# Kernel tuning notes

Measured on AMD Instinct MI355X. Metric: run time of the kernel, lower is better.

## Reference

```python
import jax, jax.numpy as jnp
import numpy as np

DIM, K, H, D, G = 1024, 4, 8, 128, 4

def rotate_half(x):
    x1, x2 = jnp.split(x, 2, axis=-1)
    return jnp.concatenate([-x2, x1], axis=-1)

def setup_inputs() -> dict:
    key = jax.random.key(0)
    ks = jax.random.split(key, 14)
    s = 0.02
    return {
        "x":  jax.random.normal(ks[0], (1, 2048, DIM), jnp.float32),
        "Wq": jax.random.normal(ks[1], (H * D, DIM), jnp.float32) * s,
        "bq": jnp.zeros((H * D,), jnp.float32),
        "Wk": jax.random.normal(ks[2], (G * D, DIM), jnp.float32) * s,
        "bk": jnp.zeros((G * D,), jnp.float32),
        "Wv": jax.random.normal(ks[3], (G * D, DIM), jnp.float32) * s,
        "bv": jnp.zeros((G * D,), jnp.float32),
        "Wo": jax.random.normal(ks[4], (DIM, H * D), jnp.float32) * s,
        "bo": jnp.zeros((DIM,), jnp.float32),
        "W1": jax.random.normal(ks[5], (DIM * 4, DIM), jnp.float32) * s,
        "b1": jnp.zeros((DIM * 4,), jnp.float32),
        "W2": jax.random.normal(ks[6], (K * DIM, DIM * 4), jnp.float32) * s,
        "b2": jnp.zeros((K * DIM,), jnp.float32),
    }

def reference(x, Wq, bq, Wk, bk, Wv, bv, Wo, bo, W1, b1, W2, b2):
    B, S, _ = x.shape
    q = (x @ Wq.T + bq).reshape(B, S, H, D).transpose(0, 2, 1, 3)  # (B,H,S,D)
    k = (x @ Wk.T + bk).reshape(B, S, G, D).transpose(0, 2, 1, 3)  # (B,G,S,D)
    v = (x @ Wv.T + bv).reshape(B, S, G, D).transpose(0, 2, 1, 3)
    # rotary embedding (same as RotaryEmbedding module)
    inv_freq = 1.0 / (10000.0 ** (jnp.arange(0, D, 2, dtype=jnp.float32) / D))
    t = jnp.arange(S, dtype=jnp.float32)
    freqs = t[:, None] * inv_freq[None, :]
    emb = jnp.concatenate([freqs, freqs], axis=-1)            # (S, D)
    cos = jnp.cos(emb)[None, None, :, :]
    sin = jnp.sin(emb)[None, None, :, :]
    q = q * cos + rotate_half(q) * sin
    k = k * cos + rotate_half(k) * sin
    # every q head attends to every kv group; softmax over j, then sum over g and j
    scores = jnp.einsum('bhid,bgjd->bhgij', q, k) / jnp.sqrt(jnp.float32(D))
    mask = jnp.triu(jnp.ones((S, S), dtype=bool), 1)
    scores = jnp.where(mask[None, None, None, :, :], -jnp.inf, scores)
    w = jax.nn.softmax(scores, axis=-1)
    attn = jnp.einsum('bhgij,bgjd->bhid', w, v)               # (B,H,S,D)
    attn = attn.transpose(0, 2, 1, 3).reshape(B, S, H * D)
    o = attn @ Wo.T + bo
    h1 = jax.nn.silu(o @ W1.T + b1)
    out = (h1 @ W2.T + b2).reshape(B, S, K, DIM)
    return out
```

## Files before the change

### kernel.cpp

```cpp
#include <hip/hip_runtime.h>
#include <hip/hip_bf16.h>

#define SEQ 2048

typedef unsigned short ushort_t;
typedef __attribute__((ext_vector_type(8))) short short8;
typedef __attribute__((ext_vector_type(4))) float f32x4;

__device__ __forceinline__ ushort_t f2bf(float f) {
    __hip_bfloat16 h = __float2bfloat16(f);
    return *reinterpret_cast<ushort_t*>(&h);
}

__device__ __forceinline__ void st(float* p, float v) { *p = v; }
__device__ __forceinline__ void st(ushort_t* p, float v) { *p = f2bf(v); }

__device__ __forceinline__ void gload16(const ushort_t* g, ushort_t* l) {
    __builtin_amdgcn_global_load_lds(
        (const __attribute__((address_space(1))) unsigned int*)g,
        (__attribute__((address_space(3))) unsigned int*)l, 16, 0, 0);
}

__global__ void cvt_bf_kernel(const float* __restrict__ s0, ushort_t* __restrict__ d0, int n0,
                              const float* __restrict__ s1, ushort_t* __restrict__ d1, int n1,
                              const float* __restrict__ s2, ushort_t* __restrict__ d2, int n2,
                              const float* __restrict__ s3, ushort_t* __restrict__ d3, int n3,
                              const float* __restrict__ s4, ushort_t* __restrict__ d4) {
    int u = blockIdx.x * 256 + threadIdx.x;
    const float* s; ushort_t* d;
    if (u < n0) { s = s0; d = d0; }
    else if ((u -= n0) < n1) { s = s1; d = d1; }
    else if ((u -= n1) < n2) { s = s2; d = d2; }
    else if ((u -= n2) < n3) { s = s3; d = d3; }
    else { u -= n3; s = s4; d = d4; }
    float4 a = ((const float4*)s)[u];
    union { ushort_t us[4]; unsigned long long ll; } pk;
    pk.us[0] = f2bf(a.x); pk.us[1] = f2bf(a.y);
    pk.us[2] = f2bf(a.z); pk.us[3] = f2bf(a.w);
    ((unsigned long long*)d)[u] = pk.ll;
}

template <bool SILU, typename TC>
__global__ __launch_bounds__(256) void mfma_gemm_kernel(
    const ushort_t* __restrict__ A, const ushort_t* __restrict__ W,
    const float* __restrict__ bias0, const float* __restrict__ bias1,
    const float* __restrict__ bias2, int sp1, int sp2,
    TC* __restrict__ C, int M, int N, int Kd, int NBX) {
    __shared__ __align__(16) ushort_t As[128 * 64];
    __shared__ __align__(16) ushort_t Bs[128 * 64];
    const int tid = threadIdx.x;
    const int w = tid >> 6, lane = tid & 63, l15 = lane & 15, quad = lane >> 4;
    const int nwg = gridDim.x;
    const int qq = nwg >> 3;
    const int bid = blockIdx.x;
    const int sw = (bid & 7) * qq + (bid >> 3);
    const int m0 = (sw / NBX) * 128, n0 = (sw % NBX) * 128;
    const int rw = (w >> 1) * 64, cw = (w & 1) * 64;
    const int rA = w * 32 + (lane >> 3);
    const int cch = ((lane & 7) ^ (lane >> 3)) * 8;

    f32x4 acc[4][4];
#pragma unroll
    for (int mt = 0; mt < 4; ++mt)
#pragma unroll
        for (int nt = 0; nt < 4; ++nt) acc[mt][nt] = (f32x4){0.f, 0.f, 0.f, 0.f};

    for (int k0 = 0; k0 < Kd; k0 += 64) {
#pragma unroll
        for (int c = 0; c < 4; ++c) {
            gload16(&A[(size_t)(m0 + rA + c * 8) * Kd + k0 + cch],
                    &As[(w * 4 + c) * 512]);
            gload16(&W[(size_t)(n0 + rA + c * 8) * Kd + k0 + cch],
                    &Bs[(w * 4 + c) * 512]);
        }
        __syncthreads();
#pragma unroll
        for (int kc = 0; kc < 2; ++kc) {
            short8 af[4], bfr[4];
#pragma unroll
            for (int mt = 0; mt < 4; ++mt) {
                int row = rw + mt * 16 + l15;
                int slot = (kc * 4 + quad) ^ (row & 7);
                af[mt] = *(const short8*)&As[row * 64 + slot * 8];
            }
#pragma unroll
            for (int nt = 0; nt < 4; ++nt) {
                int row = cw + nt * 16 + l15;
                int slot = (kc * 4 + quad) ^ (row & 7);
                bfr[nt] = *(const short8*)&Bs[row * 64 + slot * 8];
            }
#pragma unroll
            for (int mt = 0; mt < 4; ++mt)
#pragma unroll
                for (int nt = 0; nt < 4; ++nt)
                    acc[mt][nt] = __builtin_amdgcn_mfma_f32_16x16x32_bf16(
                        af[mt], bfr[nt], acc[mt][nt], 0, 0, 0);
        }
        __syncthreads();
    }
#pragma unroll
    for (int nt = 0; nt < 4; ++nt) {
        int col = n0 + cw + nt * 16 + l15;
        float bb = col < sp1 ? bias0[col]
                 : (col < sp2 ? bias1[col - sp1] : bias2[col - sp2]);
#pragma unroll
        for (int mt = 0; mt < 4; ++mt)
#pragma unroll
            for (int r = 0; r < 4; ++r) {
                int row = m0 + rw + mt * 16 + quad * 4 + r;
                float v = acc[mt][nt][r] + bb;
                if (SILU) v = v / (1.f + __expf(-v));
                st(&C[(size_t)row * N + col], v);
            }
    }
}

__global__ void rope_bf_kernel(const float* __restrict__ qkv,
                               ushort_t* __restrict__ qb, ushort_t* __restrict__ kb) {
    const int s = blockIdx.x;
    const float t = (float)s;
    const float qs = 0.08838834764831845f;
    for (int p = threadIdx.x; p < 768; p += 256) {
        int idx = p & 63;
        float invf = exp2f(-(float)idx * 0.20762050593f);
        float ang = t * invf;
        float c = cosf(ang), sn = sinf(ang);
        if (p < 512) {
            int h = p >> 6;
            const float* src = qkv + (size_t)s * 2048 + h * 128 + idx;
            ushort_t* dst = qb + (size_t)s * 1024 + h * 128 + idx;
            float x1 = src[0], x2 = src[64];
            dst[0] = f2bf((x1 * c - x2 * sn) * qs);
            dst[64] = f2bf((x2 * c + x1 * sn) * qs);
        } else {
            int h = (p - 512) >> 6;
            const float* src = qkv + (size_t)s * 2048 + 1024 + h * 128 + idx;
            ushort_t* dst = kb + (size_t)s * 512 + h * 128 + idx;
            float x1 = src[0], x2 = src[64];
            dst[0] = f2bf(x1 * c - x2 * sn);
            dst[64] = f2bf(x2 * c + x1 * sn);
        }
    }
}

__global__ void transpose_v_kernel(const float* __restrict__ qkv, ushort_t* __restrict__ vT) {
    __shared__ __align__(16) ushort_t t[64][72];
    const int s0 = blockIdx.x * 64, d0 = blockIdx.y * 64;
    const int tid = threadIdx.x;
#pragma unroll
    for (int it = 0; it < 4; ++it) {
        int u = tid + it * 256;
        int r = u >> 4, c4 = u & 15;
        float4 a = *(const float4*)&qkv[(size_t)(s0 + r) * 2048 + 1536 + d0 + c4 * 4];
        union { ushort_t us[4]; unsigned long long ll; } pk;
        pk.us[0] = f2bf(a.x); pk.us[1] = f2bf(a.y);
        pk.us[2] = f2bf(a.z); pk.us[3] = f2bf(a.w);
        *(unsigned long long*)&t[r][c4 * 4] = pk.ll;
    }
    __syncthreads();
#pragma unroll
    for (int it = 0; it < 2; ++it) {
        int u = tid + it * 256;
        int r = u >> 3, c8 = u & 7;
        short8 o;
        ushort_t* op = (ushort_t*)&o;
#pragma unroll
        for (int i = 0; i < 8; ++i) op[i] = t[c8 * 8 + i][r];
        *(short8*)&vT[(size_t)(d0 + r) * 2048 + s0 + c8 * 8] = o;
    }
}

__global__ __launch_bounds__(256, 2) void mfma_attn_kernel(
    const ushort_t* __restrict__ qb, const ushort_t* __restrict__ kb,
    const ushort_t* __restrict__ vT, float* __restrict__ part) {
    const int tid = threadIdx.x;
    const int w = tid >> 6;
    const int lane = tid & 63;
    const int l15 = lane & 15;
    const int quad = lane >> 4;
    const int bx = blockIdx.x;
    const int pr = bx >> 3;
    const int g = (bx >> 1) & 3;
    const int h = (bx & 1) * 4 + w;

    const ushort_t* vtg = vT + (size_t)g * 128 * 2048;

    __shared__ __align__(16) ushort_t Ks[64 * 128];
    __shared__ __align__(16) ushort_t Vs[128 * 64];
    __shared__ __align__(16) ushort_t P_lds[4][16][72];

#pragma unroll 1
    for (int half = 0; half < 2; ++half) {
        const int p = half ? (127 - pr) : pr;
        const int i0 = p << 4;
        const int jmax = p >> 2;
        const int rbase = (p & 3) << 4;

        short8 aq[4];
        {
            const ushort_t* qrow = qb + (size_t)(i0 + l15) * 1024 + h * 128 + quad * 8;
#pragma unroll
            for (int kc = 0; kc < 4; ++kc) aq[kc] = *(const short8*)(qrow + kc * 32);
        }
        f32x4 oacc[8];
#pragma unroll
        for (int nt = 0; nt < 8; ++nt) oacc[nt] = (f32x4){0.f, 0.f, 0.f, 0.f};
        float l_part[4] = {0.f, 0.f, 0.f, 0.f};

        short8 kreg[4], vreg[4];
#pragma unroll
        for (int it = 0; it < 4; ++it) {
            int fl = it * 256 + tid;
            int r = fl >> 4, c8 = fl & 15;
            kreg[it] = *(const short8*)&kb[(size_t)r * 512 + g * 128 + c8 * 8];
        }
#pragma unroll
        for (int it = 0; it < 4; ++it) {
            int fl = it * 256 + tid;
            int r = fl >> 3, c8 = fl & 7;
            vreg[it] = *(const short8*)&vtg[(size_t)r * 2048 + c8 * 8];
        }

        for (int jt = 0; jt <= jmax; ++jt) {
            __syncthreads();
#pragma unroll
            for (int it = 0; it < 4; ++it) {
                int fl = it * 256 + tid;
                int r = fl >> 4, c8 = fl & 15;
                *(short8*)&Ks[r * 128 + ((c8 ^ (r & 7)) * 8)] = kreg[it];
            }
#pragma unroll
            for (int it = 0; it < 4; ++it) {
                int fl = it * 256 + tid;
                int r = fl >> 3, c8 = fl & 7;
                *(short8*)&Vs[r * 64 + ((c8 ^ (r & 7)) * 8)] = vreg[it];
            }
            __syncthreads();
            if (jt < jmax) {
                const int j1 = (jt + 1) << 6;
#pragma unroll
                for (int it = 0; it < 4; ++it) {
                    int fl = it * 256 + tid;
                    int r = fl >> 4, c8 = fl & 15;
                    kreg[it] = *(const short8*)&kb[(size_t)(j1 + r) * 512 + g * 128 + c8 * 8];
                }
#pragma unroll
                for (int it = 0; it < 4; ++it) {
                    int fl = it * 256 + tid;
                    int r = fl >> 3, c8 = fl & 7;
                    vreg[it] = *(const short8*)&vtg[(size_t)r * 2048 + j1 + c8 * 8];
                }
            }
            f32x4 sacc[4];
#pragma unroll
            for (int nt = 0; nt < 4; ++nt) sacc[nt] = (f32x4){0.f, 0.f, 0.f, 0.f};
#pragma unroll
            for (int nt = 0; nt < 4; ++nt) {
                const ushort_t* krow = &Ks[(nt * 16 + l15) * 128];
                const int sw = l15 & 7;
#pragma unroll
                for (int kc = 0; kc < 4; ++kc) {
                    short8 bk = *(const short8*)(krow + (((kc * 4 + quad) ^ sw) * 8));
                    sacc[nt] = __builtin_amdgcn_mfma_f32_16x16x32_bf16(
                        aq[kc], bk, sacc[nt], 0, 0, 0);
                }
            }
            if (jt == jmax) {
#pragma unroll
                for (int nt = 0; nt < 4; ++nt) {
                    int colg = nt * 16 + l15;
#pragma unroll
                    for (int r = 0; r < 4; ++r) {
                        int rowg = rbase + quad * 4 + r;
                        if (colg > rowg) sacc[nt][r] = -1e30f;
                    }
                }
            }
#pragma unroll
            for (int nt = 0; nt < 4; ++nt)
#pragma unroll
                for (int r = 0; r < 4; ++r) {
                    float e = __expf(sacc[nt][r] - 14.f);
                    sacc[nt][r] = e;
                    l_part[r] += e;
                }
#pragma unroll
            for (int nt = 0; nt < 4; ++nt)
#pragma unroll
                for (int r = 0; r < 4; ++r)
                    P_lds[w][quad * 4 + r][nt * 16 + l15] = f2bf(sacc[nt][r]);
            asm volatile("s_waitcnt lgkmcnt(0)" ::: "memory");
            __builtin_amdgcn_sched_barrier(0);
#pragma unroll
            for (int c = 0; c < 2; ++c) {
                short8 ap = *(const short8*)&P_lds[w][l15][c * 32 + quad * 8];
#pragma unroll
                for (int nt = 0; nt < 8; ++nt) {
                    short8 bv = *(const short8*)
                        &Vs[(nt * 16 + l15) * 64 + (((c * 4 + quad) ^ (l15 & 7)) * 8)];
                    oacc[nt] = __builtin_amdgcn_mfma_f32_16x16x32_bf16(
                        ap, bv, oacc[nt], 0, 0, 0);
                }
            }
        }
#pragma unroll
        for (int r = 0; r < 4; ++r) {
            float s = l_part[r];
            s += __shfl_xor(s, 1);
            s += __shfl_xor(s, 2);
            s += __shfl_xor(s, 4);
            s += __shfl_xor(s, 8);
            float inv = 1.f / s;
            int row = i0 + quad * 4 + r;
            float* dst = part + ((size_t)g * SEQ + row) * 1024 + h * 128;
#pragma unroll
            for (int nt = 0; nt < 8; ++nt) dst[nt * 16 + l15] = oacc[nt][r] * inv;
        }
    }
}

__global__ void sum4_bf_kernel(const float* __restrict__ part, ushort_t* __restrict__ attn) {
    int idx = blockIdx.x * 256 + threadIdx.x;
    const float4* p = (const float4*)part;
    float4 a = p[idx];
    float4 b = p[idx + 524288];
    float4 c = p[idx + 2 * 524288];
    float4 d = p[idx + 3 * 524288];
    union { ushort_t u[4]; unsigned long long ll; } pk;
    pk.u[0] = f2bf(a.x + b.x + c.x + d.x);
    pk.u[1] = f2bf(a.y + b.y + c.y + d.y);
    pk.u[2] = f2bf(a.z + b.z + c.z + d.z);
    pk.u[3] = f2bf(a.w + b.w + c.w + d.w);
    *(unsigned long long*)&attn[(size_t)idx * 4] = pk.ll;
}

extern "C" void kernel_launch(void* const* d_in, const int* in_sizes, int n_in,
                              void* d_out, int out_size, void* d_ws, size_t ws_size,
                              hipStream_t stream) {
    const float* x  = (const float*)d_in[0];
    const float* Wq = (const float*)d_in[1];
    const float* bq = (const float*)d_in[2];
    const float* Wk = (const float*)d_in[3];
    const float* bk = (const float*)d_in[4];
    const float* Wv = (const float*)d_in[5];
    const float* bv = (const float*)d_in[6];
    const float* Wo = (const float*)d_in[7];
    const float* bo = (const float*)d_in[8];
    const float* W1 = (const float*)d_in[9];
    const float* b1 = (const float*)d_in[10];
    const float* W2 = (const float*)d_in[11];
    const float* b2 = (const float*)d_in[12];
    float* out = (float*)d_out;

    char* ws = (char*)d_ws;
#define MB(x) ((size_t)(x) << 20)
    float*    part    = (float*)(ws);
    ushort_t* W2_bf   = (ushort_t*)(ws);
    float*    qkv_f32 = (float*)(ws + MB(32));
    ushort_t* o_bf    = (ushort_t*)(ws + MB(32));
    ushort_t* attn_bf = (ushort_t*)(ws + MB(36));
    ushort_t* h1_bf   = (ushort_t*)(ws + MB(40));
    ushort_t* x_bf    = (ushort_t*)(ws + MB(48));
    ushort_t* q_bf    = (ushort_t*)(ws + MB(48));
    ushort_t* Wqkv_bf = (ushort_t*)(ws + MB(52));
    ushort_t* Wq_bf   = (ushort_t*)(ws + MB(52));
    ushort_t* Wk_bf   = (ushort_t*)(ws + MB(54));
    ushort_t* Wv_bf   = (ushort_t*)(ws + MB(55));
    ushort_t* k_bf    = (ushort_t*)(ws + MB(52));
    ushort_t* vT      = (ushort_t*)(ws + MB(54));
    ushort_t* Wo_bf   = (ushort_t*)(ws + MB(54));
    ushort_t* W1_bf   = (ushort_t*)(ws + MB(56));
#undef MB

    cvt_bf_kernel<<<8192, 256, 0, stream>>>(
        x, x_bf, 524288, Wq, Wq_bf, 262144, Wk, Wk_bf, 131072,
        Wv, Wv_bf, 131072, W1, W1_bf);
    mfma_gemm_kernel<false, float><<<256, 256, 0, stream>>>(
        x_bf, Wqkv_bf, bq, bk, bv, 1024, 1536, qkv_f32, SEQ, 2048, 1024, 16);
    transpose_v_kernel<<<dim3(32, 8), 256, 0, stream>>>(qkv_f32, vT);
    rope_bf_kernel<<<SEQ, 256, 0, stream>>>(qkv_f32, q_bf, k_bf);
    mfma_attn_kernel<<<512, 256, 0, stream>>>(q_bf, k_bf, vT, part);
    sum4_bf_kernel<<<2048, 256, 0, stream>>>(part, attn_bf);
    cvt_bf_kernel<<<17408, 256, 0, stream>>>(
        Wo, Wo_bf, 262144, W2, W2_bf, 4194304, W2, W2_bf, 0,
        W2, W2_bf, 0, W2, W2_bf);
    mfma_gemm_kernel<false, ushort_t><<<128, 256, 0, stream>>>(
        attn_bf, Wo_bf, bo, bo, bo, 1024, 1024, o_bf, SEQ, 1024, 1024, 8);
    mfma_gemm_kernel<true, ushort_t><<<512, 256, 0, stream>>>(
        o_bf, W1_bf, b1, b1, b1, 4096, 4096, h1_bf, SEQ, 4096, 1024, 32);
    mfma_gemm_kernel<false, float><<<512, 256, 0, stream>>>(
        h1_bf, W2_bf, b2, b2, b2, 4096, 4096, out, SEQ, 4096, 4096, 32);
}
```

Baseline: 393.8 us.

## Add triple-buffered 256x128 MFMA GEMM for MLP and fuse rope/V-transpose kernels

Adds a new 512-thread GEMM kernel with 256x128 tiles and a three-stage LDS ring filled by direct global-to-LDS loads, using explicit vmcnt waits and barriers so the loads for stage t+3 overlap the MFMA work on stage t. It is used for the two large MLP GEMMs, which are the main cost. Separately, the rope and V-transpose kernels are merged into one launch to save a kernel launch. The new GEMM uses 144KB of LDS per block with high register pressure, allowing one block per CU, and the hand-counted waitcnt values must stay in step with the number of loads issued per stage.

```diff
diff --git a/kernel.cpp b/kernel.cpp
--- a/kernel.cpp
+++ b/kernel.cpp
@@ -115,58 +115,163 @@
     }
 }
 
-__global__ void rope_bf_kernel(const float* __restrict__ qkv,
-                               ushort_t* __restrict__ qb, ushort_t* __restrict__ kb) {
-    const int s = blockIdx.x;
-    const float t = (float)s;
-    const float qs = 0.08838834764831845f;
-    for (int p = threadIdx.x; p < 768; p += 256) {
-        int idx = p & 63;
-        float invf = exp2f(-(float)idx * 0.20762050593f);
-        float ang = t * invf;
-        float c = cosf(ang), sn = sinf(ang);
-        if (p < 512) {
-            int h = p >> 6;
-            const float* src = qkv + (size_t)s * 2048 + h * 128 + idx;
-            ushort_t* dst = qb + (size_t)s * 1024 + h * 128 + idx;
-            float x1 = src[0], x2 = src[64];
-            dst[0] = f2bf((x1 * c - x2 * sn) * qs);
-            dst[64] = f2bf((x2 * c + x1 * sn) * qs);
+__device__ __forceinline__ void stage_pipe(
+    const ushort_t* __restrict__ A, const ushort_t* __restrict__ W,
+    ushort_t* Abuf, ushort_t* Bbuf, int m0, int n0, int Kd, int kk,
+    int w, int lr, int cch) {
+#pragma unroll
+    for (int cc = 0; cc < 4; ++cc)
+        gload16(&A[(size_t)(m0 + w * 32 + cc * 8 + lr) * Kd + kk + cch],
+                &Abuf[(w * 4 + cc) * 512]);
+#pragma unroll
+    for (int cc = 0; cc < 2; ++cc)
+        gload16(&W[(size_t)(n0 + w * 16 + cc * 8 + lr) * Kd + kk + cch],
+                &Bbuf[(w * 2 + cc) * 512]);
+}
+
+template <bool SILU, typename TC>
+__global__ __launch_bounds__(512) void mfma_gemm_pipe(
+    const ushort_t* __restrict__ A, const ushort_t* __restrict__ W,
+    const float* __restrict__ bias, TC* __restrict__ C,
+    int M, int N, int Kd, int NBX) {
+    __shared__ __align__(16) ushort_t Ap[3][256 * 64];
+    __shared__ __align__(16) ushort_t Bp[3][128 * 64];
+    const int tid = threadIdx.x;
+    const int w = tid >> 6, lane = tid & 63, l15 = lane & 15, quad = lane >> 4;
+    const int wm = w >> 2, wn = w & 3;
+    const int nwg = gridDim.x, qq = nwg >> 3, bid = blockIdx.x;
+    const int sw = (bid & 7) * qq + (bid >> 3);
+    const int m0 = (sw / NBX) * 256, n0 = (sw % NBX) * 128;
+    const int rw = wm * 128, cw = wn * 32;
+    const int lr = lane >> 3;
+    const int cch = ((lane & 7) ^ lr) * 8;
+    const int nt = Kd >> 6;
+
+    f32x4 acc[8][2];
+#pragma unroll
+    for (int mt = 0; mt < 8; ++mt)
+#pragma unroll
+        for (int n2 = 0; n2 < 2; ++n2) acc[mt][n2] = (f32x4){0.f, 0.f, 0.f, 0.f};
+
+    stage_pipe(A, W, Ap[0], Bp[0], m0, n0, Kd, 0, w, lr, cch);
+    stage_pipe(A, W, Ap[1], Bp[1], m0, n0, Kd, 64, w, lr, cch);
+    stage_pipe(A, W, Ap[2], Bp[2], m0, n0, Kd, 128, w, lr, cch);
+    asm volatile("s_waitcnt vmcnt(12)" ::: "memory");
+    __builtin_amdgcn_sched_barrier(0);
+    __builtin_amdgcn_s_barrier();
+
+    for (int t = 0; t < nt; ++t) {
+        const int c = t % 3;
+        const ushort_t* As = Ap[c];
+        const ushort_t* Bs = Bp[c];
+        __builtin_amdgcn_sched_barrier(0);
+        short8 bfr[2][2];
+#pragma unroll
+        for (int n2 = 0; n2 < 2; ++n2) {
+            int row = cw + n2 * 16 + l15;
+#pragma unroll
+            for (int kc = 0; kc < 2; ++kc)
+                bfr[n2][kc] = *(const short8*)
+                    &Bs[row * 64 + (((kc * 4 + quad) ^ (row & 7)) * 8)];
+        }
+#pragma unroll
+        for (int mt = 0; mt < 8; ++mt) {
+            int row = rw + mt * 16 + l15;
+            short8 a0 = *(const short8*)&As[row * 64 + (((quad) ^ (row & 7)) * 8)];
+            short8 a1 = *(const short8*)&As[row * 64 + (((4 + quad) ^ (row & 7)) * 8)];
+            __builtin_amdgcn_s_setprio(1);
+            acc[mt][0] = __builtin_amdgcn_mfma_f32_16x16x32_bf16(a0, bfr[0][0], acc[mt][0], 0, 0, 0);
+            acc[mt][0] = __builtin_amdgcn_mfma_f32_16x16x32_bf16(a1, bfr[0][1], acc[mt][0], 0, 0, 0);
+            acc[mt][1] = __builtin_amdgcn_mfma_f32_16x16x32_bf16(a0, bfr[1][0], acc[mt][1], 0, 0, 0);
+            acc[mt][1] = __builtin_amdgcn_mfma_f32_16x16x32_bf16(a1, bfr[1][1], acc[mt][1], 0, 0, 0);
+            __builtin_amdgcn_s_setprio(0);
+        }
+        if (t + 1 == nt) break;
+        __builtin_amdgcn_sched_barrier(0);
+        __builtin_amdgcn_s_barrier();
+        if (t + 3 < nt) {
+            stage_pipe(A, W, Ap[c], Bp[c], m0, n0, Kd, (t + 3) << 6, w, lr, cch);
+            asm volatile("s_waitcnt vmcnt(12)" ::: "memory");
+        } else if (t + 2 < nt) {
+            asm volatile("s_waitcnt vmcnt(6)" ::: "memory");
         } else {
-            int h = (p - 512) >> 6;
-            const float* src = qkv + (size_t)s * 2048 + 1024 + h * 128 + idx;
-            ushort_t* dst = kb + (size_t)s * 512 + h * 128 + idx;
-            float x1 = src[0], x2 = src[64];
-            dst[0] = f2bf(x1 * c - x2 * sn);
-            dst[64] = f2bf(x2 * c + x1 * sn);
-        }
-    }
-}
-
-__global__ void transpose_v_kernel(const float* __restrict__ qkv, ushort_t* __restrict__ vT) {
-    __shared__ __align__(16) ushort_t t[64][72];
-    const int s0 = blockIdx.x * 64, d0 = blockIdx.y * 64;
+            asm volatile("s_waitcnt vmcnt(0)" ::: "memory");
+        }
+        __builtin_amdgcn_sched_barrier(0);
+        __builtin_amdgcn_s_barrier();
+    }
+
+#pragma unroll
+    for (int n2 = 0; n2 < 2; ++n2) {
+        int col = n0 + cw + n2 * 16 + l15;
+        float bb = bias[col];
+#pragma unroll
+        for (int mt = 0; mt < 8; ++mt)
+#pragma unroll
+            for (int r = 0; r < 4; ++r) {
+                int row = m0 + rw + mt * 16 + quad * 4 + r;
+                float v = acc[mt][n2][r] + bb;
+                if (SILU) v = v / (1.f + __expf(-v));
+                st(&C[(size_t)row * N + col], v);
+            }
+    }
+}
+
+__global__ void prep_kernel(const float* __restrict__ qkv,
+                            ushort_t* __restrict__ qb, ushort_t* __restrict__ kb,
+                            ushort_t* __restrict__ vT) {
+    const int bx = blockIdx.x;
     const int tid = threadIdx.x;
-#pragma unroll
-    for (int it = 0; it < 4; ++it) {
-        int u = tid + it * 256;
-        int r = u >> 4, c4 = u & 15;
-        float4 a = *(const float4*)&qkv[(size_t)(s0 + r) * 2048 + 1536 + d0 + c4 * 4];
-        union { ushort_t us[4]; unsigned long long ll; } pk;
-        pk.us[0] = f2bf(a.x); pk.us[1] = f2bf(a.y);
-        pk.us[2] = f2bf(a.z); pk.us[3] = f2bf(a.w);
-        *(unsigned long long*)&t[r][c4 * 4] = pk.ll;
-    }
-    __syncthreads();
-#pragma unroll
-    for (int it = 0; it < 2; ++it) {
-        int u = tid + it * 256;
-        int r = u >> 3, c8 = u & 7;
-        short8 o;
-        ushort_t* op = (ushort_t*)&o;
-#pragma unroll
-        for (int i = 0; i < 8; ++i) op[i] = t[c8 * 8 + i][r];
-        *(short8*)&vT[(size_t)(d0 + r) * 2048 + s0 + c8 * 8] = o;
+    if (bx < 2048) {
+        const int s = bx;
+        const float t = (float)s;
+        const float qs = 0.08838834764831845f;
+        for (int p = tid; p < 768; p += 256) {
+            int idx = p & 63;
+            float invf = exp2f(-(float)idx * 0.20762050593f);
+            float ang = t * invf;
+            float c = cosf(ang), sn = sinf(ang);
+            if (p < 512) {
+                int h = p >> 6;
+                const float* src = qkv + (size_t)s * 2048 + h * 128 + idx;
+                ushort_t* dst = qb + (size_t)s * 1024 + h * 128 + idx;
+                float x1 = src[0], x2 = src[64];
+                dst[0] = f2bf((x1 * c - x2 * sn) * qs);
+                dst[64] = f2bf((x2 * c + x1 * sn) * qs);
+            } else {
+                int h = (p - 512) >> 6;
+                const float* src = qkv + (size_t)s * 2048 + 1024 + h * 128 + idx;
+                ushort_t* dst = kb + (size_t)s * 512 + h * 128 + idx;
+                float x1 = src[0], x2 = src[64];
+                dst[0] = f2bf(x1 * c - x2 * sn);
+                dst[64] = f2bf(x2 * c + x1 * sn);
+            }
+        }
+    } else {
+        __shared__ __align__(16) ushort_t t[64][72];
+        const int u = bx - 2048;
+        const int s0 = (u & 31) * 64, d0 = (u >> 5) * 64;
+#pragma unroll
+        for (int it = 0; it < 4; ++it) {
+            int uu = tid + it * 256;
+            int r = uu >> 4, c4 = uu & 15;
+            float4 a = *(const float4*)&qkv[(size_t)(s0 + r) * 2048 + 1536 + d0 + c4 * 4];
+            union { ushort_t us[4]; unsigned long long ll; } pk;
+            pk.us[0] = f2bf(a.x); pk.us[1] = f2bf(a.y);
+            pk.us[2] = f2bf(a.z); pk.us[3] = f2bf(a.w);
+            *(unsigned long long*)&t[r][c4 * 4] = pk.ll;
+        }
+        __syncthreads();
+#pragma unroll
+        for (int it = 0; it < 2; ++it) {
+            int uu = tid + it * 256;
+            int r = uu >> 3, c8 = uu & 7;
+            short8 o;
+            ushort_t* op = (ushort_t*)&o;
+#pragma unroll
+            for (int i = 0; i < 8; ++i) op[i] = t[c8 * 8 + i][r];
+            *(short8*)&vT[(size_t)(d0 + r) * 2048 + s0 + c8 * 8] = o;
+        }
     }
 }
 
@@ -377,8 +482,7 @@
         Wv, Wv_bf, 131072, W1, W1_bf);
     mfma_gemm_kernel<false, float><<<256, 256, 0, stream>>>(
         x_bf, Wqkv_bf, bq, bk, bv, 1024, 1536, qkv_f32, SEQ, 2048, 1024, 16);
-    transpose_v_kernel<<<dim3(32, 8), 256, 0, stream>>>(qkv_f32, vT);
-    rope_bf_kernel<<<SEQ, 256, 0, stream>>>(qkv_f32, q_bf, k_bf);
+    prep_kernel<<<2304, 256, 0, stream>>>(qkv_f32, q_bf, k_bf, vT);
     mfma_attn_kernel<<<512, 256, 0, stream>>>(q_bf, k_bf, vT, part);
     sum4_bf_kernel<<<2048, 256, 0, stream>>>(part, attn_bf);
     cvt_bf_kernel<<<17408, 256, 0, stream>>>(
@@ -386,8 +490,8 @@
         W2, W2_bf, 0, W2, W2_bf);
     mfma_gemm_kernel<false, ushort_t><<<128, 256, 0, stream>>>(
         attn_bf, Wo_bf, bo, bo, bo, 1024, 1024, o_bf, SEQ, 1024, 1024, 8);
-    mfma_gemm_kernel<true, ushort_t><<<512, 256, 0, stream>>>(
-        o_bf, W1_bf, b1, b1, b1, 4096, 4096, h1_bf, SEQ, 4096, 1024, 32);
-    mfma_gemm_kernel<false, float><<<512, 256, 0, stream>>>(
-        h1_bf, W2_bf, b2, b2, b2, 4096, 4096, out, SEQ, 4096, 4096, 32);
-}
+    mfma_gemm_pipe<true, ushort_t><<<256, 512, 0, stream>>>(
+        o_bf, W1_bf, b1, h1_bf, SEQ, 4096, 1024, 32);
+    mfma_gemm_pipe<false, float><<<256, 512, 0, stream>>>(
+        h1_bf, W2_bf, b2, out, SEQ, 4096, 4096, 32);
+}
```

Measured after the change: 413.0 us. 4.9% more time.

## Fuse rope and V transpose into the QKV GEMM epilogue

Applied to the files above, without the earlier changes.

Replaces the QKV GEMM plus the separate transpose and rope kernels with one kernel. Its epilogue stages each 64-row half tile in LDS, then writes bf16 rotated q/k and transposed v directly. This removes the fp32 qkv intermediate round trip through memory and two launches. In exchange it adds extra LDS staging and syncs in the epilogue, and recomputes sin/cos per tile.

```diff
diff --git a/kernel.cpp b/kernel.cpp
--- a/kernel.cpp
+++ b/kernel.cpp
@@ -43,9 +43,8 @@
 template <bool SILU, typename TC>
 __global__ __launch_bounds__(256) void mfma_gemm_kernel(
     const ushort_t* __restrict__ A, const ushort_t* __restrict__ W,
-    const float* __restrict__ bias0, const float* __restrict__ bias1,
-    const float* __restrict__ bias2, int sp1, int sp2,
-    TC* __restrict__ C, int M, int N, int Kd, int NBX) {
+    const float* __restrict__ bias, TC* __restrict__ C,
+    int M, int N, int Kd, int NBX) {
     __shared__ __align__(16) ushort_t As[128 * 64];
     __shared__ __align__(16) ushort_t Bs[128 * 64];
     const int tid = threadIdx.x;
@@ -101,8 +100,7 @@
 #pragma unroll
     for (int nt = 0; nt < 4; ++nt) {
         int col = n0 + cw + nt * 16 + l15;
-        float bb = col < sp1 ? bias0[col]
-                 : (col < sp2 ? bias1[col - sp1] : bias2[col - sp2]);
+        float bb = bias[col];
 #pragma unroll
         for (int mt = 0; mt < 4; ++mt)
 #pragma unroll
@@ -115,58 +113,125 @@
     }
 }
 
-__global__ void rope_bf_kernel(const float* __restrict__ qkv,
-                               ushort_t* __restrict__ qb, ushort_t* __restrict__ kb) {
-    const int s = blockIdx.x;
-    const float t = (float)s;
-    const float qs = 0.08838834764831845f;
-    for (int p = threadIdx.x; p < 768; p += 256) {
-        int idx = p & 63;
-        float invf = exp2f(-(float)idx * 0.20762050593f);
-        float ang = t * invf;
-        float c = cosf(ang), sn = sinf(ang);
-        if (p < 512) {
-            int h = p >> 6;
-            const float* src = qkv + (size_t)s * 2048 + h * 128 + idx;
-            ushort_t* dst = qb + (size_t)s * 1024 + h * 128 + idx;
-            float x1 = src[0], x2 = src[64];
-            dst[0] = f2bf((x1 * c - x2 * sn) * qs);
-            dst[64] = f2bf((x2 * c + x1 * sn) * qs);
+__global__ __launch_bounds__(256) void mfma_qkv_kernel(
+    const ushort_t* __restrict__ A, const ushort_t* __restrict__ W,
+    const float* __restrict__ bq, const float* __restrict__ bk,
+    const float* __restrict__ bv,
+    ushort_t* __restrict__ q_bf, ushort_t* __restrict__ k_bf,
+    ushort_t* __restrict__ vT, int Kd) {
+    __shared__ __align__(16) ushort_t smem[2 * 128 * 64];
+    ushort_t* As = smem;
+    ushort_t* Bs = smem + 128 * 64;
+    float* Cs = (float*)smem;
+    const int tid = threadIdx.x;
+    const int w = tid >> 6, lane = tid & 63, l15 = lane & 15, quad = lane >> 4;
+    const int nwg = gridDim.x;
+    const int qq = nwg >> 3;
+    const int bid = blockIdx.x;
+    const int sw = (bid & 7) * qq + (bid >> 3);
+    const int m0 = (sw >> 4) * 128, n0 = (sw & 15) * 128;
+    const int rw = (w >> 1) * 64, cw = (w & 1) * 64;
+    const int rA = w * 32 + (lane >> 3);
+    const int cch = ((lane & 7) ^ (lane >> 3)) * 8;
+
+    f32x4 acc[4][4];
+#pragma unroll
+    for (int mt = 0; mt < 4; ++mt)
+#pragma unroll
+        for (int nt = 0; nt < 4; ++nt) acc[mt][nt] = (f32x4){0.f, 0.f, 0.f, 0.f};
+
+    for (int k0 = 0; k0 < Kd; k0 += 64) {
+#pragma unroll
+        for (int c = 0; c < 4; ++c) {
+            gload16(&A[(size_t)(m0 + rA + c * 8) * Kd + k0 + cch],
+                    &As[(w * 4 + c) * 512]);
+            gload16(&W[(size_t)(n0 + rA + c * 8) * Kd + k0 + cch],
+                    &Bs[(w * 4 + c) * 512]);
+        }
+        __syncthreads();
+#pragma unroll
+        for (int kc = 0; kc < 2; ++kc) {
+            short8 af[4], bfr[4];
+#pragma unroll
+            for (int mt = 0; mt < 4; ++mt) {
+                int row = rw + mt * 16 + l15;
+                int slot = (kc * 4 + quad) ^ (row & 7);
+                af[mt] = *(const short8*)&As[row * 64 + slot * 8];
+            }
+#pragma unroll
+            for (int nt = 0; nt < 4; ++nt) {
+                int row = cw + nt * 16 + l15;
+                int slot = (kc * 4 + quad) ^ (row & 7);
+                bfr[nt] = *(const short8*)&Bs[row * 64 + slot * 8];
+            }
+#pragma unroll
+            for (int mt = 0; mt < 4; ++mt)
+#pragma unroll
+                for (int nt = 0; nt < 4; ++nt)
+                    acc[mt][nt] = __builtin_amdgcn_mfma_f32_16x16x32_bf16(
+                        af[mt], bfr[nt], acc[mt][nt], 0, 0, 0);
+        }
+        __syncthreads();
+    }
+
+    const bool isq = n0 < 1024;
+    const bool isv = n0 >= 1536;
+    const int hhw = w >> 1;
+    union S8 { ushort_t u[8]; short8 v; };
+#pragma unroll 1
+    for (int hh = 0; hh < 2; ++hh) {
+        if (hhw == hh) {
+#pragma unroll
+            for (int nt = 0; nt < 4; ++nt) {
+                int col = cw + nt * 16 + l15;
+                int gcol = n0 + col;
+                float bb = gcol < 1024 ? bq[gcol]
+                         : (gcol < 1536 ? bk[gcol - 1024] : bv[gcol - 1536]);
+#pragma unroll
+                for (int mt = 0; mt < 4; ++mt)
+#pragma unroll
+                    for (int r = 0; r < 4; ++r)
+                        Cs[(mt * 16 + quad * 4 + r) * 128 + col] = acc[mt][nt][r] + bb;
+            }
+        }
+        __syncthreads();
+        const int srow0 = m0 + hh * 64;
+        if (!isv) {
+            const int hd = (n0 >> 7) & 7;
+            const float sc = isq ? 0.08838834764831845f : 1.f;
+            for (int uu = tid; uu < 512; uu += 256) {
+                int row = uu >> 3, ic = uu & 7;
+                int s = srow0 + row;
+                float t = (float)s;
+                S8 o1, o2;
+#pragma unroll
+                for (int j = 0; j < 8; ++j) {
+                    int idx = ic * 8 + j;
+                    float invf = exp2f(-(float)idx * 0.20762050593f);
+                    float ang = t * invf;
+                    float c = cosf(ang), sn = sinf(ang);
+                    float x1 = Cs[row * 128 + idx];
+                    float x2 = Cs[row * 128 + idx + 64];
+                    o1.u[j] = f2bf((x1 * c - x2 * sn) * sc);
+                    o2.u[j] = f2bf((x2 * c + x1 * sn) * sc);
+                }
+                ushort_t* dst = isq ? (q_bf + (size_t)s * 1024 + hd * 128)
+                                    : (k_bf + (size_t)s * 512 + hd * 128);
+                *(short8*)(dst + ic * 8) = o1.v;
+                *(short8*)(dst + ic * 8 + 64) = o2.v;
+            }
         } else {
-            int h = (p - 512) >> 6;
-            const float* src = qkv + (size_t)s * 2048 + 1024 + h * 128 + idx;
-            ushort_t* dst = kb + (size_t)s * 512 + h * 128 + idx;
-            float x1 = src[0], x2 = src[64];
-            dst[0] = f2bf(x1 * c - x2 * sn);
-            dst[64] = f2bf(x2 * c + x1 * sn);
-        }
-    }
-}
-
-__global__ void transpose_v_kernel(const float* __restrict__ qkv, ushort_t* __restrict__ vT) {
-    __shared__ __align__(16) ushort_t t[64][72];
-    const int s0 = blockIdx.x * 64, d0 = blockIdx.y * 64;
-    const int tid = threadIdx.x;
-#pragma unroll
-    for (int it = 0; it < 4; ++it) {
-        int u = tid + it * 256;
-        int r = u >> 4, c4 = u & 15;
-        float4 a = *(const float4*)&qkv[(size_t)(s0 + r) * 2048 + 1536 + d0 + c4 * 4];
-        union { ushort_t us[4]; unsigned long long ll; } pk;
-        pk.us[0] = f2bf(a.x); pk.us[1] = f2bf(a.y);
-        pk.us[2] = f2bf(a.z); pk.us[3] = f2bf(a.w);
-        *(unsigned long long*)&t[r][c4 * 4] = pk.ll;
-    }
-    __syncthreads();
-#pragma unroll
-    for (int it = 0; it < 2; ++it) {
-        int u = tid + it * 256;
-        int r = u >> 3, c8 = u & 7;
-        short8 o;
-        ushort_t* op = (ushort_t*)&o;
-#pragma unroll
-        for (int i = 0; i < 8; ++i) op[i] = t[c8 * 8 + i][r];
-        *(short8*)&vT[(size_t)(d0 + r) * 2048 + s0 + c8 * 8] = o;
+            const int g = (n0 - 1536) >> 7;
+            for (int uu = tid; uu < 1024; uu += 256) {
+                int d = uu >> 3, sc8 = uu & 7;
+                S8 o;
+#pragma unroll
+                for (int j = 0; j < 8; ++j)
+                    o.u[j] = f2bf(Cs[(sc8 * 8 + j) * 128 + d]);
+                *(short8*)&vT[(size_t)(g * 128 + d) * 2048 + srow0 + sc8 * 8] = o.v;
+            }
+        }
+        __syncthreads();
     }
 }
 
@@ -356,38 +421,35 @@
 #define MB(x) ((size_t)(x) << 20)
     float*    part    = (float*)(ws);
     ushort_t* W2_bf   = (ushort_t*)(ws);
-    float*    qkv_f32 = (float*)(ws + MB(32));
+    ushort_t* x_bf    = (ushort_t*)(ws + MB(32));
     ushort_t* o_bf    = (ushort_t*)(ws + MB(32));
+    ushort_t* Wqkv_bf = (ushort_t*)(ws + MB(36));
+    ushort_t* Wq_bf   = (ushort_t*)(ws + MB(36));
+    ushort_t* Wk_bf   = (ushort_t*)(ws + MB(38));
+    ushort_t* Wv_bf   = (ushort_t*)(ws + MB(39));
     ushort_t* attn_bf = (ushort_t*)(ws + MB(36));
+    ushort_t* q_bf    = (ushort_t*)(ws + MB(40));
+    ushort_t* k_bf    = (ushort_t*)(ws + MB(44));
+    ushort_t* vT      = (ushort_t*)(ws + MB(46));
+    ushort_t* Wo_bf   = (ushort_t*)(ws + MB(48));
     ushort_t* h1_bf   = (ushort_t*)(ws + MB(40));
-    ushort_t* x_bf    = (ushort_t*)(ws + MB(48));
-    ushort_t* q_bf    = (ushort_t*)(ws + MB(48));
-    ushort_t* Wqkv_bf = (ushort_t*)(ws + MB(52));
-    ushort_t* Wq_bf   = (ushort_t*)(ws + MB(52));
-    ushort_t* Wk_bf   = (ushort_t*)(ws + MB(54));
-    ushort_t* Wv_bf   = (ushort_t*)(ws + MB(55));
-    ushort_t* k_bf    = (ushort_t*)(ws + MB(52));
-    ushort_t* vT      = (ushort_t*)(ws + MB(54));
-    ushort_t* Wo_bf   = (ushort_t*)(ws + MB(54));
     ushort_t* W1_bf   = (ushort_t*)(ws + MB(56));
 #undef MB
 
     cvt_bf_kernel<<<8192, 256, 0, stream>>>(
         x, x_bf, 524288, Wq, Wq_bf, 262144, Wk, Wk_bf, 131072,
         Wv, Wv_bf, 131072, W1, W1_bf);
-    mfma_gemm_kernel<false, float><<<256, 256, 0, stream>>>(
-        x_bf, Wqkv_bf, bq, bk, bv, 1024, 1536, qkv_f32, SEQ, 2048, 1024, 16);
-    transpose_v_kernel<<<dim3(32, 8), 256, 0, stream>>>(qkv_f32, vT);
-    rope_bf_kernel<<<SEQ, 256, 0, stream>>>(qkv_f32, q_bf, k_bf);
+    mfma_qkv_kernel<<<256, 256, 0, stream>>>(
+        x_bf, Wqkv_bf, bq, bk, bv, q_bf, k_bf, vT, 1024);
     mfma_attn_kernel<<<512, 256, 0, stream>>>(q_bf, k_bf, vT, part);
     sum4_bf_kernel<<<2048, 256, 0, stream>>>(part, attn_bf);
     cvt_bf_kernel<<<17408, 256, 0, stream>>>(
         Wo, Wo_bf, 262144, W2, W2_bf, 4194304, W2, W2_bf, 0,
         W2, W2_bf, 0, W2, W2_bf);
     mfma_gemm_kernel<false, ushort_t><<<128, 256, 0, stream>>>(
-        attn_bf, Wo_bf, bo, bo, bo, 1024, 1024, o_bf, SEQ, 1024, 1024, 8);
+        attn_bf, Wo_bf, bo, o_bf, SEQ, 1024, 1024, 8);
     mfma_gemm_kernel<true, ushort_t><<<512, 256, 0, stream>>>(
-        o_bf, W1_bf, b1, b1, b1, 4096, 4096, h1_bf, SEQ, 4096, 1024, 32);
+        o_bf, W1_bf, b1, h1_bf, SEQ, 4096, 1024, 32);
     mfma_gemm_kernel<false, float><<<512, 256, 0, stream>>>(
-        h1_bf, W2_bf, b2, b2, b2, 4096, 4096, out, SEQ, 4096, 4096, 32);
-}
+        h1_bf, W2_bf, b2, out, SEQ, 4096, 4096, 32);
+}
```

New measurement: 382.7 us. -2.8%, faster.
